# Kernel optimization log

Hardware: AMD Instinct MI355X
Metric: run time of the kernel (lower is better)

Reference implementation:

```python
import jax, jax.numpy as jnp
import numpy as np

E = 1024
H = 16
DH = E // H
EPS = 1e-8
GRAM_W = 1.5


def _gram_scores(q, k1, k2):
    # q: [BH, L, D], k1/k2: [BH, S, D] -> [BH, L, S]
    ll = jnp.sum(q * q, -1)[:, :, None]          # [BH, L, 1]
    vv = jnp.sum(k1 * k1, -1)[:, None, :]        # [BH, 1, S]
    aa = jnp.sum(k2 * k2, -1)[:, None, :]
    va = jnp.sum(k1 * k2, -1)[:, None, :]
    lv = jnp.einsum('bld,bsd->bls', q, k1)
    la = jnp.einsum('bld,bsd->bls', q, k2)
    det = ll * (vv * aa - va * va) - lv * (lv * aa - la * va) + la * (lv * va - la * vv)
    return -jnp.sqrt(jnp.clip(det, EPS, None))


def setup_inputs() -> dict:
    key = jax.random.key(0)
    ks = jax.random.split(key, 20)
    L, B, S = 512, 4, 1024
    inp = {
        'query': jax.random.normal(ks[0], (L, B, E), jnp.float32),
        'mod1': jax.random.normal(ks[1], (S, B, E), jnp.float32),
        'mod2': jax.random.normal(ks[2], (S, B, E), jnp.float32),
    }
    # Linear params stored as [in, out] (y = x @ W + b), 8 linears
    names = ['q', 'k1', 'k2', 'v1', 'v2', 'g1', 'g2', 'o']
    for i, n in enumerate(names):
        inp[n + '_w'] = jax.random.normal(ks[3 + 2 * i], (E, E), jnp.float32) * 0.02
        inp[n + '_b'] = jax.random.normal(ks[4 + 2 * i], (E,), jnp.float32) * 0.02
    return inp


def reference(query, mod1, mod2,
              q_w, q_b, k1_w, k1_b, k2_w, k2_b, v1_w, v1_b, v2_w, v2_b,
              g1_w, g1_b, g2_w, g2_b, o_w, o_b):
    L, B, _ = query.shape
    S = mod1.shape[0]
    scaling = DH ** -0.5

    def lin(x, w, b):
        return x @ w + b

    def split_heads(x, n):  # [n, B, E] -> [B*H, n, DH]
        return x.reshape(n, B * H, DH).transpose(1, 0, 2)

    q = split_heads(lin(query, q_w, q_b) * scaling, L)
    k1 = split_heads(lin(mod1, k1_w, k1_b), S)
    k2 = split_heads(lin(mod2, k2_w, k2_b), S)
    v1 = split_heads(lin(mod1, v1_w, v1_b), S)
    v2 = split_heads(lin(mod2, v2_w, v2_b), S)

    w1 = jnp.einsum('bld,bsd->bls', q, k1)
    w2 = jnp.einsum('bld,bsd->bls', q, k2)
    gram = _gram_scores(q, k1, k2)
    logits = GRAM_W * gram + w1 + w2          # [BH, L, S]
    attn = jax.nn.softmax(logits, axis=-1)

    def merge_heads(x):  # [B*H, L, DH] -> [L, B, E]
        return x.transpose(1, 0, 2).reshape(L, B, E)

    out1 = merge_heads(jnp.einsum('bls,bsd->bld', attn, v1))
    out2 = merge_heads(jnp.einsum('bls,bsd->bld', attn, v2))
    gate1 = jax.nn.sigmoid(lin(query, g1_w, g1_b))
    gate2 = jax.nn.sigmoid(lin(query, g2_w, g2_b))
    attn_output = lin((out1 * gate1 + out2 * gate2) / 2.0, o_w, o_b)
    avg_weights = attn.reshape(B, H, L, S).mean(axis=1)
    return attn_output, avg_weights
```

## Files before the change

### kernel.cpp

```cpp
#include <hip/hip_runtime.h>
#include <cstddef>
#include <cstdint>

typedef unsigned short ushort_t;
typedef unsigned int uint_t;
typedef __attribute__((ext_vector_type(8))) short short8;
typedef __attribute__((ext_vector_type(4))) float f32x4;

#define EDIM 1024
#define NHEAD 16
#define HDIM 64
#define NB 4
#define LQ 512
#define SK 1024
#define BHD 64

__device__ __forceinline__ ushort_t f2b(float f) {
    uint_t u = __float_as_uint(f);
    return (ushort_t)((u + 0x7fffu + ((u >> 16) & 1u)) >> 16);
}
__device__ __forceinline__ float b2f(ushort_t b) {
    return __uint_as_float(((uint_t)b) << 16);
}

__device__ __forceinline__ void gload_lds16(const void* g, void* l) {
    __builtin_amdgcn_global_load_lds((const __attribute__((address_space(1))) void*)g,
                                     (__attribute__((address_space(3))) void*)l, 16, 0, 0);
}

struct MegaArgs {
    const ushort_t *qx, *m1h, *m1l, *m2h, *m2l;
    const ushort_t *Wqg, *Wkv1, *Wkv2, *Wk1l, *Wk2l;
    const float *q_b, *k1_b, *k2_b, *v1_b, *v2_b, *g1_b, *g2_b;
    float *K1f, *K2f;
    ushort_t *V1b, *V2b, *Qb, *G1b, *G2b;
};

__global__ __launch_bounds__(256, 2)
void mega_gemm(MegaArgs a)
{
    __shared__ ushort_t As[128 * 64];
    __shared__ ushort_t Bs[128 * 64];
    const int tid = threadIdx.x;
    const int wave = tid >> 6, lane = tid & 63;
    const int ln = lane & 15, lq = lane >> 4;
    const int wm = wave & 1, wn = wave >> 1;
    const int mrl = lane >> 3;
    const int lswz = (lane & 7) ^ mrl;

    const int id = blockIdx.x;
    f32x4 zero = {0.f, 0.f, 0.f, 0.f};

    if (id < 512) {
        const int kind = id >> 8;
        const int t = id & 255;
        const int u = t >> 3;
        const int col0 = (u >> 2) * 128;
        const int row0 = ((t & 7) * 4 + (u & 3)) * 128;
        const ushort_t* Ah  = kind ? a.m2h : a.m1h;
        const ushort_t* Alo = kind ? a.m2l : a.m1l;
        const ushort_t* Bh  = kind ? a.Wkv2 : a.Wkv1;
        const ushort_t* Blo = kind ? a.Wk2l : a.Wk1l;
        const float* bias = kind ? a.k2_b : a.k1_b;

        f32x4 acc[4][4];
#pragma unroll
        for (int i = 0; i < 4; ++i)
#pragma unroll
            for (int j = 0; j < 4; ++j) acc[i][j] = zero;

        const int ksub = (lswz & 3) * 8;
        const ushort_t* Asrc = (lswz & 4) ? Alo : Ah;
        const ushort_t* Bsrc = (lswz & 4) ? Blo : Bh;

        for (int kk = 0; kk < 1024; kk += 32) {
            __syncthreads();
#pragma unroll
            for (int j = 0; j < 4; ++j) {
                const int mr = (wave * 4 + j) * 8 + mrl;
                gload_lds16(Asrc + (size_t)(row0 + mr) * 1024 + kk + ksub,
                            (void*)(As + (wave * 4 + j) * 512));
                gload_lds16(Bsrc + (size_t)(col0 + mr) * 1024 + kk + ksub,
                            (void*)(Bs + (wave * 4 + j) * 512));
            }
            __syncthreads();
            short8 ah[4], alv[4], bh[4], blv[4];
#pragma unroll
            for (int i = 0; i < 4; ++i) {
                const int ml = wm * 64 + i * 16 + ln;
                const int pa = (lq ^ (ml & 7)) * 8;
                ah[i]  = *(const short8*)(As + ml * 64 + pa);
                alv[i] = *(const short8*)(As + ml * 64 + (pa ^ 32));
                const int nl = wn * 64 + i * 16 + ln;
                const int pb = (lq ^ (nl & 7)) * 8;
                bh[i]  = *(const short8*)(Bs + nl * 64 + pb);
                blv[i] = *(const short8*)(Bs + nl * 64 + (pb ^ 32));
            }
#pragma unroll
            for (int i = 0; i < 4; ++i)
#pragma unroll
                for (int j = 0; j < 4; ++j)
                    acc[i][j] = __builtin_amdgcn_mfma_f32_16x16x32_bf16(ah[i], bh[j], acc[i][j], 0, 0, 0);
#pragma unroll
            for (int i = 0; i < 4; ++i)
#pragma unroll
                for (int j = 0; j < 4; ++j)
                    acc[i][j] = __builtin_amdgcn_mfma_f32_16x16x32_bf16(ah[i], blv[j], acc[i][j], 0, 0, 0);
#pragma unroll
            for (int i = 0; i < 4; ++i)
#pragma unroll
                for (int j = 0; j < 4; ++j)
                    acc[i][j] = __builtin_amdgcn_mfma_f32_16x16x32_bf16(alv[i], bh[j], acc[i][j], 0, 0, 0);
        }

        float* Y = kind ? a.K2f : a.K1f;
#pragma unroll
        for (int i = 0; i < 4; ++i) {
#pragma unroll
            for (int r = 0; r < 4; ++r) {
                const int row = row0 + wm * 64 + i * 16 + lq * 4 + r;
#pragma unroll
                for (int j = 0; j < 4; ++j) {
                    const int col = col0 + wn * 64 + j * 16 + ln;
                    const float v = acc[i][j][r] + bias[col];
                    const int s = row >> 2, b = row & 3, h = col >> 6, d = col & 63;
                    Y[(((size_t)(b * 16 + h)) * 1024 + s) * 64 + d] = v;
                }
            }
        }
        return;
    }

    int kind, row0, col0;
    const ushort_t *A, *B;
    const float* bias;
    if (id < 1024) {
        int t = id - 512; kind = 2 + (t >> 8); t &= 255;
        const int u = t >> 3;
        col0 = (u >> 2) * 128;
        row0 = ((t & 7) * 4 + (u & 3)) * 128;
        A = (kind == 2) ? a.m1h : a.m2h;
        B = ((kind == 2) ? a.Wkv1 : a.Wkv2) + (size_t)1024 * 1024;
        bias = (kind == 2) ? a.v1_b : a.v2_b;
    } else {
        const int t = id - 1024; kind = 4;
        const int u = t >> 3;
        const int c = (t & 7) * 3 + (u >> 4);
        const int rr = u & 15;
        col0 = c * 128; row0 = rr * 128;
        A = a.qx; B = a.Wqg;
        const int seg = c >> 3;
        bias = (seg == 0) ? a.q_b : ((seg == 1) ? a.g1_b : a.g2_b);
    }

    f32x4 acc[4][4];
#pragma unroll
    for (int i = 0; i < 4; ++i)
#pragma unroll
        for (int j = 0; j < 4; ++j) acc[i][j] = zero;

    for (int kk = 0; kk < 1024; kk += 64) {
        __syncthreads();
#pragma unroll
        for (int j = 0; j < 4; ++j) {
            const int mr = (wave * 4 + j) * 8 + mrl;
            gload_lds16(A + (size_t)(row0 + mr) * 1024 + kk + lswz * 8,
                        (void*)(As + (wave * 4 + j) * 512));
            gload_lds16(B + (size_t)(col0 + mr) * 1024 + kk + lswz * 8,
                        (void*)(Bs + (wave * 4 + j) * 512));
        }
        __syncthreads();
#pragma unroll
        for (int sub = 0; sub < 2; ++sub) {
            short8 af[4], bfv[4];
#pragma unroll
            for (int i = 0; i < 4; ++i) {
                const int ml = wm * 64 + i * 16 + ln;
                af[i] = *(const short8*)(As + ml * 64 + (((sub * 4 + lq) ^ (ml & 7)) * 8));
                const int nl = wn * 64 + i * 16 + ln;
                bfv[i] = *(const short8*)(Bs + nl * 64 + (((sub * 4 + lq) ^ (nl & 7)) * 8));
            }
#pragma unroll
            for (int i = 0; i < 4; ++i)
#pragma unroll
                for (int j = 0; j < 4; ++j)
                    acc[i][j] = __builtin_amdgcn_mfma_f32_16x16x32_bf16(af[i], bfv[j], acc[i][j], 0, 0, 0);
        }
    }

#pragma unroll
    for (int i = 0; i < 4; ++i) {
#pragma unroll
        for (int r = 0; r < 4; ++r) {
            const int row = row0 + wm * 64 + i * 16 + lq * 4 + r;
#pragma unroll
            for (int j = 0; j < 4; ++j) {
                const int col = col0 + wn * 64 + j * 16 + ln;
                const int lc = col & 1023;
                float v = acc[i][j][r] + bias[lc];
                if (kind <= 3) {
                    const int s = row >> 2, b = row & 3, h = lc >> 6, d = lc & 63;
                    ushort_t* Y = (kind == 2) ? a.V1b : a.V2b;
                    Y[(((size_t)(b * 16 + h)) * 1024 + s) * 64 + d] = f2b(v);
                } else {
                    const int seg = col >> 10;
                    if (seg == 0) {
                        v *= 0.125f;
                        const int s = row >> 2, b = row & 3, h = lc >> 6, d = lc & 63;
                        a.Qb[(((size_t)(b * 16 + h)) * 512 + s) * 64 + d] = f2b(v);
                    } else {
                        v = 1.0f / (1.0f + __expf(-v));
                        ushort_t* Y = (seg == 1) ? a.G1b : a.G2b;
                        Y[(size_t)row * 1024 + lc] = f2b(v);
                    }
                }
            }
        }
    }
}

struct CastArgs {
    const float* q; const float* m1; const float* m2;
    ushort_t* qx; ushort_t* m1h; ushort_t* m1l; ushort_t* m2h; ushort_t* m2l;
    const float* wsrc[8];
    ushort_t* whi[8];
    ushort_t* wlo[8];
};

__global__ __launch_bounds__(256)
void casts_kernel(CastArgs a)
{
    __shared__ float T[64][65];
    const int id = blockIdx.x;
    const int tid = threadIdx.x;
    if (id < 1024) {
        const size_t i = ((size_t)id * 256 + tid) * 8;
        float4 x = *(const float4*)(a.q + i);
        float4 y = *(const float4*)(a.q + i + 4);
        ushort_t o[8] = {f2b(x.x), f2b(x.y), f2b(x.z), f2b(x.w), f2b(y.x), f2b(y.y), f2b(y.z), f2b(y.w)};
        *(uint4*)( (void*)(a.qx + i) ) = *(const uint4*)o;
    } else if (id < 5120) {
        const int t = id - 1024;
        const int which = t >> 11;
        const float* x = which ? a.m2 : a.m1;
        ushort_t* yh = which ? a.m2h : a.m1h;
        ushort_t* yl = which ? a.m2l : a.m1l;
        const size_t i = ((size_t)(t & 2047) * 256 + tid) * 8;
        float v[8];
        *(float4*)v = *(const float4*)(x + i);
        *(float4*)(v + 4) = *(const float4*)(x + i + 4);
        ushort_t oh[8], ol[8];
#pragma unroll
        for (int k = 0; k < 8; ++k) {
            oh[k] = f2b(v[k]);
            ol[k] = f2b(v[k] - b2f(oh[k]));
        }
        *(uint4*)( (void*)(yh + i) ) = *(const uint4*)oh;
        *(uint4*)( (void*)(yl + i) ) = *(const uint4*)ol;
    } else {
        const int t = id - 5120;
        const int z = t >> 8, x = t & 15, y = (t >> 4) & 15;
        const float* W = a.wsrc[z];
        ushort_t* Th = a.whi[z];
        ushort_t* Tl = a.wlo[z];
        const int k0 = x * 64, n0 = y * 64;
        const int r = tid >> 2, cg = (tid & 3) * 16;
#pragma unroll
        for (int u = 0; u < 4; ++u) {
            float4 v = *(const float4*)(W + (size_t)(k0 + r) * 1024 + n0 + cg + u * 4);
            T[r][cg + u * 4 + 0] = v.x; T[r][cg + u * 4 + 1] = v.y;
            T[r][cg + u * 4 + 2] = v.z; T[r][cg + u * 4 + 3] = v.w;
        }
        __syncthreads();
        ushort_t oh[16], ol[16];
#pragma unroll
        for (int u = 0; u < 16; ++u) {
            float v = T[cg + u][r];
            oh[u] = f2b(v);
            ol[u] = f2b(v - b2f(oh[u]));
        }
        ushort_t* dh = Th + (size_t)(n0 + r) * 1024 + k0 + cg;
        *(uint4*)( (void*)dh ) = *(const uint4*)oh;
        *(uint4*)( (void*)(dh + 8) ) = *(const uint4*)(oh + 8);
        if (Tl) {
            ushort_t* dl = Tl + (size_t)(n0 + r) * 1024 + k0 + cg;
            *(uint4*)( (void*)dl ) = *(const uint4*)ol;
            *(uint4*)( (void*)(dl + 8) ) = *(const uint4*)(ol + 8);
        }
    }
}

__global__ __launch_bounds__(256)
void prep_kernel(const float* __restrict__ K1f, const float* __restrict__ K2f,
                 ushort_t* __restrict__ K1b, ushort_t* __restrict__ K2b,
                 float* __restrict__ vv, float* __restrict__ aa,
                 float* __restrict__ va2, float* __restrict__ gg,
                 const ushort_t* __restrict__ Qb, float* __restrict__ ll,
                 const ushort_t* __restrict__ V1b, const ushort_t* __restrict__ V2b,
                 ushort_t* __restrict__ V1t, ushort_t* __restrict__ V2t)
{
    __shared__ float T[64][65];
    const int id = blockIdx.x;
    const int tid = threadIdx.x;
    const int wave = tid >> 6, lane = tid & 63;
    if (id < 16384) {
        const int row = id * 4 + wave;
        const float x1 = K1f[(size_t)row * 64 + lane];
        const float x2 = K2f[(size_t)row * 64 + lane];
        K1b[(size_t)row * 64 + lane] = f2b(x1);
        K2b[(size_t)row * 64 + lane] = f2b(x2);
        float s1 = x1 * x1, s2 = x2 * x2, s3 = x1 * x2;
#pragma unroll
        for (int o = 1; o < 64; o <<= 1) {
            s1 += __shfl_xor(s1, o);
            s2 += __shfl_xor(s2, o);
            s3 += __shfl_xor(s3, o);
        }
        if (lane == 0) {
            vv[row] = s1; aa[row] = s2;
            va2[row] = 2.0f * s3;
            gg[row] = s1 * s2 - s3 * s3;
        }
    } else if (id < 24576) {
        const int row = (id - 16384) * 4 + wave;
        const float x = b2f(Qb[(size_t)row * 64 + lane]);
        float s = x * x;
#pragma unroll
        for (int o = 1; o < 64; o <<= 1) s += __shfl_xor(s, o);
        if (lane == 0) ll[row] = s;
    } else {
        const int t = id - 24576;
        const int z = t >> 10, bh = (t >> 4) & 63, s0 = (t & 15) * 64;
        const ushort_t* S = z ? V2b : V1b;
        ushort_t* D = z ? V2t : V1t;
        const int r = tid >> 2, cg = (tid & 3) * 16;
        ushort_t buf[16];
        const ushort_t* sp = S + ((size_t)bh * 1024 + s0 + r) * 64 + cg;
        *(uint4*)buf = *(const uint4*)sp;
        *(uint4*)(buf + 8) = *(const uint4*)(sp + 8);
#pragma unroll
        for (int u = 0; u < 16; ++u) T[r][cg + u] = b2f(buf[u]);
        __syncthreads();
        ushort_t o[16];
#pragma unroll
        for (int u = 0; u < 16; ++u) o[u] = f2b(T[cg + u][r]);
        ushort_t* d = D + ((size_t)bh * 64 + r) * 1024 + s0 + cg;
        *(uint4*)( (void*)d ) = *(const uint4*)o;
        *(uint4*)( (void*)(d + 8) ) = *(const uint4*)(o + 8);
    }
}

__global__ __launch_bounds__(256, 2)
void attn_fused(const ushort_t* __restrict__ Qb, const ushort_t* __restrict__ K1b,
                const ushort_t* __restrict__ K2b, const float* __restrict__ ll,
                const float* __restrict__ vv, const float* __restrict__ aa,
                const float* __restrict__ va2, const float* __restrict__ gg,
                ushort_t* __restrict__ attn)
{
    __shared__ ushort_t Qs[64 * 64];
    __shared__ ushort_t K1s[128 * 64];
    __shared__ ushort_t K2s[128 * 64];
    __shared__ float vvS[1024], aaS[1024], vaS[1024], ggS[1024], llS[64];
    const int tid = threadIdx.x;
    const int wave = tid >> 6, lane = tid & 63;
    const int ln = lane & 15, lq = lane >> 4;
    const int mrl = lane >> 3;
    const int cswz = (lane & 7) ^ mrl;

    const int id = blockIdx.x;
    const int bh = (id & 7) * 8 + ((id >> 3) & 7);
    const int l0 = (id >> 6) * 64;

    for (int i = tid; i < 1024; i += 256) {
        vvS[i] = vv[(size_t)bh * 1024 + i];
        aaS[i] = aa[(size_t)bh * 1024 + i];
        vaS[i] = va2[(size_t)bh * 1024 + i];
        ggS[i] = gg[(size_t)bh * 1024 + i];
    }
    if (tid < 64) llS[tid] = ll[(size_t)bh * 512 + l0 + tid];
#pragma unroll
    for (int j = 0; j < 2; ++j) {
        const int mr = (wave * 2 + j) * 8 + mrl;
        gload_lds16(Qb + ((size_t)bh * 512 + l0 + mr) * 64 + cswz * 8,
                    (void*)(Qs + (wave * 2 + j) * 512));
    }

    const int ml = wave * 16 + ln;

    auto tile_logits = [&](int s0, float lgt[8][4]) {
        __syncthreads();
#pragma unroll
        for (int j = 0; j < 4; ++j) {
            const int mr = (wave * 4 + j) * 8 + mrl;
            gload_lds16(K1b + ((size_t)bh * 1024 + s0 + mr) * 64 + cswz * 8,
                        (void*)(K1s + (wave * 4 + j) * 512));
            gload_lds16(K2b + ((size_t)bh * 1024 + s0 + mr) * 64 + cswz * 8,
                        (void*)(K2s + (wave * 4 + j) * 512));
        }
        __syncthreads();
        f32x4 zero = {0.f, 0.f, 0.f, 0.f};
        f32x4 lv[8], la[8];
#pragma unroll
        for (int j = 0; j < 8; ++j) { lv[j] = zero; la[j] = zero; }
#pragma unroll
        for (int sub = 0; sub < 2; ++sub) {
            const short8 qf = *(const short8*)(Qs + ml * 64 + (((sub * 4 + lq) ^ (ml & 7)) * 8));
#pragma unroll
            for (int j = 0; j < 8; ++j) {
                const int nl = j * 16 + ln;
                const short8 k1f = *(const short8*)(K1s + nl * 64 + (((sub * 4 + lq) ^ (nl & 7)) * 8));
                const short8 k2f = *(const short8*)(K2s + nl * 64 + (((sub * 4 + lq) ^ (nl & 7)) * 8));
                lv[j] = __builtin_amdgcn_mfma_f32_16x16x32_bf16(qf, k1f, lv[j], 0, 0, 0);
                la[j] = __builtin_amdgcn_mfma_f32_16x16x32_bf16(qf, k2f, la[j], 0, 0, 0);
            }
        }
#pragma unroll
        for (int j = 0; j < 8; ++j) {
            const int c = s0 + j * 16 + ln;
            const float VV = vvS[c], AA = aaS[c], VA2 = vaS[c], GB = ggS[c];
#pragma unroll
            for (int r = 0; r < 4; ++r) {
                const float LL = llS[wave * 16 + lq * 4 + r];
                const float LV = lv[j][r], LA = la[j][r];
                float det = LL * GB;
                det = fmaf(-AA, LV * LV, det);
                det = fmaf(VA2, LV * LA, det);
                det = fmaf(-VV, LA * LA, det);
                det = fmaxf(det, 1e-8f);
                lgt[j][r] = (LV + LA) - 1.5f * sqrtf(det);
            }
        }
    };

    float m_run[4], s_run[4];
#pragma unroll
    for (int r = 0; r < 4; ++r) { m_run[r] = -3.0e38f; s_run[r] = 0.f; }

    for (int s0 = 0; s0 < 1024; s0 += 128) {
        float lgt[8][4];
        tile_logits(s0, lgt);
        float tmax[4];
#pragma unroll
        for (int r = 0; r < 4; ++r) tmax[r] = -3.0e38f;
#pragma unroll
        for (int j = 0; j < 8; ++j)
#pragma unroll
            for (int r = 0; r < 4; ++r) tmax[r] = fmaxf(tmax[r], lgt[j][r]);
#pragma unroll
        for (int r = 0; r < 4; ++r) {
#pragma unroll
            for (int o = 1; o < 16; o <<= 1) tmax[r] = fmaxf(tmax[r], __shfl_xor(tmax[r], o));
        }
#pragma unroll
        for (int r = 0; r < 4; ++r) {
            const float mn = fmaxf(m_run[r], tmax[r]);
            const float sc = __expf(m_run[r] - mn);
            float ps = 0.f;
#pragma unroll
            for (int j = 0; j < 8; ++j) ps += __expf(lgt[j][r] - mn);
            s_run[r] = s_run[r] * sc + ps;
            m_run[r] = mn;
        }
    }
    float inv[4];
#pragma unroll
    for (int r = 0; r < 4; ++r) {
        float s = s_run[r];
#pragma unroll
        for (int o = 1; o < 16; o <<= 1) s += __shfl_xor(s, o);
        inv[r] = 1.0f / s;
    }

    for (int s0 = 0; s0 < 1024; s0 += 128) {
        float lgt[8][4];
        tile_logits(s0, lgt);
#pragma unroll
        for (int j = 0; j < 8; ++j) {
            const int c = s0 + j * 16 + ln;
#pragma unroll
            for (int r = 0; r < 4; ++r) {
                const float p = __expf(lgt[j][r] - m_run[r]) * inv[r];
                attn[((size_t)bh * 512 + l0 + wave * 16 + lq * 4 + r) * 1024 + c] = f2b(p);
            }
        }
    }
}

__global__ __launch_bounds__(256, 2)
void pv_gate_kernel(const ushort_t* __restrict__ attn, const ushort_t* __restrict__ V1t,
                    const ushort_t* __restrict__ V2t, const ushort_t* __restrict__ G1,
                    const ushort_t* __restrict__ G2, ushort_t* __restrict__ tmpb,
                    float* __restrict__ avg)
{
    __shared__ ushort_t Ps[128 * 64];
    __shared__ ushort_t V1s[64 * 64];
    __shared__ ushort_t V2s[64 * 64];
    const int tid = threadIdx.x;

    if (blockIdx.x >= 256) {
        const int t = blockIdx.x - 256;
        const int b = t >> 9, l = t & 511;
        const int c0 = tid * 4;
        float s0_ = 0.f, s1_ = 0.f, s2_ = 0.f, s3_ = 0.f;
#pragma unroll
        for (int h = 0; h < 16; ++h) {
            const ushort_t* p = attn + (((size_t)(b * 16 + h)) * 512 + l) * 1024 + c0;
            ushort_t u[4];
            *(uint2*)u = *(const uint2*)p;
            s0_ += b2f(u[0]); s1_ += b2f(u[1]); s2_ += b2f(u[2]); s3_ += b2f(u[3]);
        }
        float4 o = {s0_ * 0.0625f, s1_ * 0.0625f, s2_ * 0.0625f, s3_ * 0.0625f};
        *(float4*)(avg + ((size_t)(b * 512 + l)) * 1024 + c0) = o;
        return;
    }

    const int wave = tid >> 6, lane = tid & 63;
    const int ln = lane & 15, lq = lane >> 4;
    const int bh = blockIdx.x >> 2;
    const int l0 = (blockIdx.x & 3) * 128;
    const int cswz = (lane & 7) ^ ((lane >> 3) & 7);
    const int mrl = lane >> 3;
    const int bq = bh >> 4, h = bh & 15;

    f32x4 zero = {0.f, 0.f, 0.f, 0.f};
    f32x4 acc1[2][4], acc2[2][4];
#pragma unroll
    for (int i = 0; i < 2; ++i)
#pragma unroll
        for (int j = 0; j < 4; ++j) { acc1[i][j] = zero; acc2[i][j] = zero; }

    for (int s0 = 0; s0 < 1024; s0 += 64) {
        __syncthreads();
#pragma unroll
        for (int j = 0; j < 4; ++j) {
            const int mr = (wave * 4 + j) * 8 + mrl;
            gload_lds16(attn + ((size_t)bh * 512 + l0 + mr) * 1024 + s0 + cswz * 8,
                        (void*)(Ps + (wave * 4 + j) * 512));
        }
#pragma unroll
        for (int j = 0; j < 2; ++j) {
            const int mv = (wave * 2 + j) * 8 + mrl;
            gload_lds16(V1t + ((size_t)bh * 64 + mv) * 1024 + s0 + cswz * 8,
                        (void*)(V1s + (wave * 2 + j) * 512));
            gload_lds16(V2t + ((size_t)bh * 64 + mv) * 1024 + s0 + cswz * 8,
                        (void*)(V2s + (wave * 2 + j) * 512));
        }
        __syncthreads();
#pragma unroll
        for (int sub = 0; sub < 2; ++sub) {
            short8 af[2], b1f[4], b2f_[4];
#pragma unroll
            for (int i = 0; i < 2; ++i) {
                const int ml = wave * 32 + i * 16 + ln;
                af[i] = *(const short8*)(Ps + ml * 64 + (((sub * 4 + lq) ^ (ml & 7)) * 8));
            }
#pragma unroll
            for (int j = 0; j < 4; ++j) {
                const int nl = j * 16 + ln;
                b1f[j] = *(const short8*)(V1s + nl * 64 + (((sub * 4 + lq) ^ (nl & 7)) * 8));
                b2f_[j] = *(const short8*)(V2s + nl * 64 + (((sub * 4 + lq) ^ (nl & 7)) * 8));
            }
#pragma unroll
            for (int i = 0; i < 2; ++i)
#pragma unroll
                for (int j = 0; j < 4; ++j) {
                    acc1[i][j] = __builtin_amdgcn_mfma_f32_16x16x32_bf16(af[i], b1f[j], acc1[i][j], 0, 0, 0);
                    acc2[i][j] = __builtin_amdgcn_mfma_f32_16x16x32_bf16(af[i], b2f_[j], acc2[i][j], 0, 0, 0);
                }
        }
    }

#pragma unroll
    for (int i = 0; i < 2; ++i) {
#pragma unroll
        for (int r = 0; r < 4; ++r) {
            const int l = l0 + wave * 32 + i * 16 + lq * 4 + r;
#pragma unroll
            for (int j = 0; j < 4; ++j) {
                const int d = j * 16 + ln;
                const size_t addr = ((size_t)l * 4 + bq) * 1024 + h * 64 + d;
                const float v = 0.5f * (acc1[i][j][r] * b2f(G1[addr]) + acc2[i][j][r] * b2f(G2[addr]));
                tmpb[addr] = f2b(v);
            }
        }
    }
}

__global__ __launch_bounds__(256, 2)
void gemm_o64(const ushort_t* __restrict__ A, const ushort_t* __restrict__ B,
              const float* __restrict__ bias, float* __restrict__ Y)
{
    __shared__ ushort_t As[64 * 64];
    __shared__ ushort_t Bs[128 * 64];
    const int tid = threadIdx.x;
    const int wave = tid >> 6, lane = tid & 63;
    const int ln = lane & 15, lq = lane >> 4;
    const int row0 = blockIdx.y * 64, col0 = blockIdx.x * 128;
    const int wm = wave & 1, wn = wave >> 1;
    const int cswz = (lane & 7) ^ ((lane >> 3) & 7);
    const int mrl = lane >> 3;

    f32x4 zero = {0.f, 0.f, 0.f, 0.f};
    f32x4 acc[2][4];
#pragma unroll
    for (int i = 0; i < 2; ++i)
#pragma unroll
        for (int j = 0; j < 4; ++j) acc[i][j] = zero;

    for (int kk = 0; kk < 1024; kk += 64) {
        __syncthreads();
#pragma unroll
        for (int j = 0; j < 2; ++j) {
            const int mr = (wave * 2 + j) * 8 + mrl;
            gload_lds16(A + (size_t)(row0 + mr) * 1024 + kk + cswz * 8,
                        (void*)(As + (wave * 2 + j) * 512));
        }
#pragma unroll
        for (int j = 0; j < 4; ++j) {
            const int mr = (wave * 4 + j) * 8 + mrl;
            gload_lds16(B + (size_t)(col0 + mr) * 1024 + kk + cswz * 8,
                        (void*)(Bs + (wave * 4 + j) * 512));
        }
        __syncthreads();
#pragma unroll
        for (int sub = 0; sub < 2; ++sub) {
            short8 af[2], bfv[4];
#pragma unroll
            for (int i = 0; i < 2; ++i) {
                const int ml = wm * 32 + i * 16 + ln;
                af[i] = *(const short8*)(As + ml * 64 + (((sub * 4 + lq) ^ (ml & 7)) * 8));
            }
#pragma unroll
            for (int j = 0; j < 4; ++j) {
                const int nl = wn * 64 + j * 16 + ln;
                bfv[j] = *(const short8*)(Bs + nl * 64 + (((sub * 4 + lq) ^ (nl & 7)) * 8));
            }
#pragma unroll
            for (int i = 0; i < 2; ++i)
#pragma unroll
                for (int j = 0; j < 4; ++j)
                    acc[i][j] = __builtin_amdgcn_mfma_f32_16x16x32_bf16(af[i], bfv[j], acc[i][j], 0, 0, 0);
        }
    }

#pragma unroll
    for (int i = 0; i < 2; ++i) {
#pragma unroll
        for (int r = 0; r < 4; ++r) {
            const int row = row0 + wm * 32 + i * 16 + lq * 4 + r;
#pragma unroll
            for (int j = 0; j < 4; ++j) {
                const int col = col0 + wn * 64 + j * 16 + ln;
                Y[(size_t)row * 1024 + col] = acc[i][j][r] + bias[col];
            }
        }
    }
}

extern "C" void kernel_launch(void* const* d_in, const int* in_sizes, int n_in,
                              void* d_out, int out_size, void* d_ws, size_t ws_size,
                              hipStream_t stream)
{
    const float* query = (const float*)d_in[0];
    const float* mod1  = (const float*)d_in[1];
    const float* mod2  = (const float*)d_in[2];
    const float* q_w  = (const float*)d_in[3];  const float* q_b  = (const float*)d_in[4];
    const float* k1_w = (const float*)d_in[5];  const float* k1_b = (const float*)d_in[6];
    const float* k2_w = (const float*)d_in[7];  const float* k2_b = (const float*)d_in[8];
    const float* v1_w = (const float*)d_in[9];  const float* v1_b = (const float*)d_in[10];
    const float* v2_w = (const float*)d_in[11]; const float* v2_b = (const float*)d_in[12];
    const float* g1_w = (const float*)d_in[13]; const float* g1_b = (const float*)d_in[14];
    const float* g2_w = (const float*)d_in[15]; const float* g2_b = (const float*)d_in[16];
    const float* o_w  = (const float*)d_in[17]; const float* o_b  = (const float*)d_in[18];
    float* out = (float*)d_out;

    const size_t MB = 1u << 20;
    char* w = (char*)d_ws;
    ushort_t* Wqg  = (ushort_t*)(w + 0 * MB);
    ushort_t* Wkv1 = (ushort_t*)(w + 6 * MB);
    ushort_t* Wkv2 = (ushort_t*)(w + 10 * MB);
    ushort_t* Wo   = (ushort_t*)(w + 14 * MB);
    ushort_t* Wk1l = (ushort_t*)(w + 16 * MB);
    ushort_t* Wk2l = (ushort_t*)(w + 18 * MB);
    ushort_t* qx   = (ushort_t*)(w + 20 * MB);
    ushort_t* tmpb = qx;
    ushort_t* Qb   = (ushort_t*)(w + 24 * MB);
    ushort_t* K1b  = (ushort_t*)(w + 28 * MB);
    ushort_t* K2b  = (ushort_t*)(w + 36 * MB);
    ushort_t* V1t  = (ushort_t*)(w + 44 * MB);
    ushort_t* V2t  = (ushort_t*)(w + 52 * MB);
    ushort_t* G1b  = (ushort_t*)(w + 60 * MB);
    ushort_t* G2b  = (ushort_t*)(w + 64 * MB);
    float* ll  = (float*)(w + 68 * MB);
    float* vv  = (float*)(w + 68 * MB + 256 * 1024);
    float* aa  = (float*)(w + 68 * MB + 512 * 1024);
    float* va2 = (float*)(w + 68 * MB + 768 * 1024);
    float* gg  = (float*)(w + 68 * MB + 1024 * 1024);
    ushort_t* attn = (ushort_t*)(w + 78 * MB);
    ushort_t* m1h = (ushort_t*)(w + 78 * MB);
    ushort_t* m2h = (ushort_t*)(w + 86 * MB);
    ushort_t* m1l = (ushort_t*)(w + 94 * MB);
    ushort_t* m2l = (ushort_t*)(w + 102 * MB);
    float* K1f = (float*)(w + 110 * MB);
    float* K2f = (float*)(w + 126 * MB);
    ushort_t* V1b = (ushort_t*)(w + 142 * MB);
    ushort_t* V2b = (ushort_t*)(w + 150 * MB);

    CastArgs ca;
    ca.q = query; ca.m1 = mod1; ca.m2 = mod2;
    ca.qx = qx; ca.m1h = m1h; ca.m1l = m1l; ca.m2h = m2h; ca.m2l = m2l;
    const float* srcs[8] = {q_w, g1_w, g2_w, k1_w, v1_w, k2_w, v2_w, o_w};
    ushort_t* his[8] = {Wqg, Wqg + (size_t)1024 * 1024, Wqg + (size_t)2048 * 1024,
                        Wkv1, Wkv1 + (size_t)1024 * 1024, Wkv2, Wkv2 + (size_t)1024 * 1024, Wo};
    ushort_t* los[8] = {nullptr, nullptr, nullptr, Wk1l, nullptr, Wk2l, nullptr, nullptr};
    for (int i = 0; i < 8; ++i) { ca.wsrc[i] = srcs[i]; ca.whi[i] = his[i]; ca.wlo[i] = los[i]; }
    casts_kernel<<<7168, 256, 0, stream>>>(ca);

    MegaArgs ma;
    ma.qx = qx; ma.m1h = m1h; ma.m1l = m1l; ma.m2h = m2h; ma.m2l = m2l;
    ma.Wqg = Wqg; ma.Wkv1 = Wkv1; ma.Wkv2 = Wkv2; ma.Wk1l = Wk1l; ma.Wk2l = Wk2l;
    ma.q_b = q_b; ma.k1_b = k1_b; ma.k2_b = k2_b; ma.v1_b = v1_b; ma.v2_b = v2_b;
    ma.g1_b = g1_b; ma.g2_b = g2_b;
    ma.K1f = K1f; ma.K2f = K2f; ma.V1b = V1b; ma.V2b = V2b;
    ma.Qb = Qb; ma.G1b = G1b; ma.G2b = G2b;
    mega_gemm<<<1408, 256, 0, stream>>>(ma);

    prep_kernel<<<26624, 256, 0, stream>>>(K1f, K2f, K1b, K2b, vv, aa, va2, gg,
                                           Qb, ll, V1b, V2b, V1t, V2t);

    attn_fused<<<512, 256, 0, stream>>>(Qb, K1b, K2b, ll, vv, aa, va2, gg, attn);

    pv_gate_kernel<<<2304, 256, 0, stream>>>(attn, V1t, V2t, G1b, G2b, tmpb,
                                             out + (size_t)LQ * NB * EDIM);

    gemm_o64<<<dim3(8, 32), 256, 0, stream>>>(tmpb, Wo, o_b, out);
}
```

Measured before the change: 387.4 us.

## Cache bf16 unnormalized probabilities in registers instead of recomputing logits

The attention-score kernel used to make two passes over the keys, recomputing the QK MFMAs and the Gram determinant in the second pass to write normalized probabilities. It now makes one pass: it stores each tile's exp values as packed bf16 in registers (128 uint per thread) together with that tile's running max, then rescales by exp(m_tile - m_final)/sum when writing out. This removes the second round of K loads and MFMAs, and it also switches to exp2 with a prescaled log2(e). The cost is much higher register pressure, which risks spills or lower occupancy under launch_bounds(256,2), plus an extra bf16 rounding step that is applied before the final scale.

```diff
diff --git a/kernel.cpp b/kernel.cpp
--- a/kernel.cpp
+++ b/kernel.cpp
@@ -366,6 +366,7 @@
     const int ln = lane & 15, lq = lane >> 4;
     const int mrl = lane >> 3;
     const int cswz = (lane & 7) ^ mrl;
+    const float L2E = 1.44269504f;
 
     const int id = blockIdx.x;
     const int bh = (id & 7) * 8 + ((id >> 3) & 7);
@@ -387,7 +388,15 @@
 
     const int ml = wave * 16 + ln;
 
-    auto tile_logits = [&](int s0, float lgt[8][4]) {
+    float m_run[4], s_run[4];
+#pragma unroll
+    for (int r = 0; r < 4; ++r) { m_run[r] = -3.0e38f; s_run[r] = 0.f; }
+    uint_t pp[8][8][2];
+    float mt[8][4];
+
+#pragma unroll
+    for (int t = 0; t < 8; ++t) {
+        const int s0 = t * 128;
         __syncthreads();
 #pragma unroll
         for (int j = 0; j < 4; ++j) {
@@ -414,6 +423,7 @@
                 la[j] = __builtin_amdgcn_mfma_f32_16x16x32_bf16(qf, k2f, la[j], 0, 0, 0);
             }
         }
+        float lgt[8][4];
 #pragma unroll
         for (int j = 0; j < 8; ++j) {
             const int c = s0 + j * 16 + ln;
@@ -430,20 +440,11 @@
                 lgt[j][r] = (LV + LA) - 1.5f * sqrtf(det);
             }
         }
-    };
-
-    float m_run[4], s_run[4];
-#pragma unroll
-    for (int r = 0; r < 4; ++r) { m_run[r] = -3.0e38f; s_run[r] = 0.f; }
-
-    for (int s0 = 0; s0 < 1024; s0 += 128) {
-        float lgt[8][4];
-        tile_logits(s0, lgt);
         float tmax[4];
 #pragma unroll
-        for (int r = 0; r < 4; ++r) tmax[r] = -3.0e38f;
-#pragma unroll
-        for (int j = 0; j < 8; ++j)
+        for (int r = 0; r < 4; ++r) tmax[r] = lgt[0][r];
+#pragma unroll
+        for (int j = 1; j < 8; ++j)
 #pragma unroll
             for (int r = 0; r < 4; ++r) tmax[r] = fmaxf(tmax[r], lgt[j][r]);
 #pragma unroll
@@ -451,17 +452,32 @@
 #pragma unroll
             for (int o = 1; o < 16; o <<= 1) tmax[r] = fmaxf(tmax[r], __shfl_xor(tmax[r], o));
         }
+        float mn[4], nm[4], ps[4];
 #pragma unroll
         for (int r = 0; r < 4; ++r) {
-            const float mn = fmaxf(m_run[r], tmax[r]);
-            const float sc = __expf(m_run[r] - mn);
-            float ps = 0.f;
-#pragma unroll
-            for (int j = 0; j < 8; ++j) ps += __expf(lgt[j][r] - mn);
-            s_run[r] = s_run[r] * sc + ps;
-            m_run[r] = mn;
-        }
-    }
+            mn[r] = fmaxf(m_run[r], tmax[r]);
+            nm[r] = -mn[r] * L2E;
+            ps[r] = 0.f;
+        }
+#pragma unroll
+        for (int j = 0; j < 8; ++j) {
+            float p[4];
+#pragma unroll
+            for (int r = 0; r < 4; ++r) {
+                p[r] = exp2f(fmaf(lgt[j][r], L2E, nm[r]));
+                ps[r] += p[r];
+            }
+            pp[t][j][0] = (uint_t)f2b(p[0]) | ((uint_t)f2b(p[1]) << 16);
+            pp[t][j][1] = (uint_t)f2b(p[2]) | ((uint_t)f2b(p[3]) << 16);
+        }
+#pragma unroll
+        for (int r = 0; r < 4; ++r) {
+            s_run[r] = s_run[r] * __expf(m_run[r] - mn[r]) + ps[r];
+            m_run[r] = mn[r];
+            mt[t][r] = mn[r];
+        }
+    }
+
     float inv[4];
 #pragma unroll
     for (int r = 0; r < 4; ++r) {
@@ -471,17 +487,20 @@
         inv[r] = 1.0f / s;
     }
 
-    for (int s0 = 0; s0 < 1024; s0 += 128) {
-        float lgt[8][4];
-        tile_logits(s0, lgt);
+    const size_t rb = (size_t)bh * 512 + l0 + wave * 16 + lq * 4;
+#pragma unroll
+    for (int t = 0; t < 8; ++t) {
+        float c[4];
+#pragma unroll
+        for (int r = 0; r < 4; ++r) c[r] = __expf(mt[t][r] - m_run[r]) * inv[r];
 #pragma unroll
         for (int j = 0; j < 8; ++j) {
-            const int c = s0 + j * 16 + ln;
-#pragma unroll
-            for (int r = 0; r < 4; ++r) {
-                const float p = __expf(lgt[j][r] - m_run[r]) * inv[r];
-                attn[((size_t)bh * 512 + l0 + wave * 16 + lq * 4 + r) * 1024 + c] = f2b(p);
-            }
+            const int col = t * 128 + j * 16 + ln;
+            const uint_t u0 = pp[t][j][0], u1 = pp[t][j][1];
+            attn[(rb + 0) * 1024 + col] = f2b(__uint_as_float(u0 << 16) * c[0]);
+            attn[(rb + 1) * 1024 + col] = f2b(__uint_as_float(u0 & 0xffff0000u) * c[1]);
+            attn[(rb + 2) * 1024 + col] = f2b(__uint_as_float(u1 << 16) * c[2]);
+            attn[(rb + 3) * 1024 + col] = f2b(__uint_as_float(u1 & 0xffff0000u) * c[3]);
         }
     }
 }
```

After: 564.1 us. +45.6%, slower.
